# Kernel optimization log

Measured on AMD Instinct MI355X. Metric: run time of the kernel, lower is better.

Reference implementation:

```python
import jax, jax.numpy as jnp
import numpy as np

CHUNK = 512
LR = 0.001  # fast-weight learning_rate


def setup_inputs() -> dict:
    key = jax.random.key(0)
    k1, k2, k3, k4 = jax.random.split(key, 4)
    B, S, H, F = 4, 4096, 1024, 4096
    x = jax.random.normal(k1, (B, S, H), dtype=jnp.float32)
    w0 = jax.random.normal(k2, (H, F), dtype=jnp.float32) * 0.02
    w1 = jax.random.normal(k3, (F, H), dtype=jnp.float32) * 0.02
    w2 = jax.random.normal(k4, (H, F), dtype=jnp.float32) * 0.02
    return {"x": x, "w0": w0, "w1": w1, "w2": w2}


def _fast_weight(xc, a0, a1, a2):
    # SwiGLU fast-weight MLP (LaCT-style): [B,C,H] -> [B,C,H]
    h = jax.nn.silu(jnp.einsum('bch,hf->bcf', xc, a0)) * jnp.einsum('bch,hf->bcf', xc, a2)
    return jnp.einsum('bcf,fh->bch', h, a1)


def reference(x, w0, w1, w2):
    B, S, H = x.shape
    nC = S // CHUNK
    # [nC, B, CHUNK, H] so scan iterates over chunks
    xc = x.reshape(B, nC, CHUNK, H).transpose(1, 0, 2, 3)

    def step(carry, x_chunk):
        a0, a1, a2, acc_loss = carry
        out = _fast_weight(x_chunk, a0, a1, a2)
        chunk_loss = jnp.mean((out - x_chunk) ** 2)
        decay = 1.0 - LR * chunk_loss  # per-chunk scalar weight decay
        return (a0 * decay, a1 * decay, a2 * decay, acc_loss + chunk_loss), out

    init = (w0, w1, w2, jnp.float32(0.0))
    (_, _, _, total_loss), outs = jax.lax.scan(step, init, xc)
    output = outs.transpose(1, 0, 2, 3).reshape(B, S, H)
    return output, total_loss / nC
```

## Files before the change

kernel.cpp:

```cpp
#include <hip/hip_runtime.h>

typedef float f32x4 __attribute__((ext_vector_type(4)));
typedef short bf16x8 __attribute__((ext_vector_type(8)));
typedef unsigned short u16;

#define B_SZ 4
#define S_SZ 4096
#define H_SZ 1024
#define F_SZ 4096
#define CHUNK_SZ 512
#define NCHUNK 8
#define MCH 2048
#define LRATE 0.001f
#define NSPLIT 4

__device__ __forceinline__ u16 f2bf(float f) {
  unsigned u = __float_as_uint(f);
  u += 0x7FFFu + ((u >> 16) & 1u);
  return (u16)(u >> 16);
}
__device__ __forceinline__ float bf2f(u16 u) {
  return __uint_as_float(((unsigned)u) << 16);
}

__device__ __forceinline__ void gload_lds16(const void* g, void* l) {
  __builtin_amdgcn_global_load_lds(
      (const __attribute__((address_space(1))) unsigned int*)g,
      (__attribute__((address_space(3))) unsigned int*)l, 16, 0, 0);
}


__global__ __launch_bounds__(256) void k_init(float* scal) {
  if (threadIdx.x == 0) { scal[0] = 1.f; scal[1] = 0.f; }
}

__global__ __launch_bounds__(256) void k_cvt_x(const float* __restrict__ x,
                                               u16* __restrict__ xb) {
  size_t i = ((size_t)blockIdx.x * 256 + threadIdx.x) * 8;
  float4 v0 = *(const float4*)(x + i);
  float4 v1 = *(const float4*)(x + i + 4);
  union { u16 u[8]; bf16x8 v; } o;
  o.u[0] = f2bf(v0.x); o.u[1] = f2bf(v0.y); o.u[2] = f2bf(v0.z); o.u[3] = f2bf(v0.w);
  o.u[4] = f2bf(v1.x); o.u[5] = f2bf(v1.y); o.u[6] = f2bf(v1.z); o.u[7] = f2bf(v1.w);
  *(bf16x8*)(xb + i) = o.v;
}

__global__ __launch_bounds__(256) void k_transpose_cvt(const float* __restrict__ W,
                                                       u16* __restrict__ Wt,
                                                       int R, int C) {
  __shared__ float tile[32][33];
  int tx = threadIdx.x & 31, ty = threadIdx.x >> 5;
  int r0 = blockIdx.y << 5, c0 = blockIdx.x << 5;
#pragma unroll
  for (int i = 0; i < 4; i++)
    tile[ty + i * 8][tx] = W[(size_t)(r0 + ty + i * 8) * C + c0 + tx];
  __syncthreads();
#pragma unroll
  for (int i = 0; i < 4; i++)
    Wt[(size_t)(c0 + ty + i * 8) * R + r0 + tx] = f2bf(tile[tx][ty + i * 8]);
}

__global__ __launch_bounds__(256, 2) void k_gemm_gu(
    const u16* __restrict__ xb,
    const u16* __restrict__ w0t,
    const u16* __restrict__ w2t,
    u16* __restrict__ hbuf,
    const float* __restrict__ scal, int chunk) {
  __shared__ __align__(16) u16 sA[128 * 64];
  __shared__ __align__(16) u16 sB0[128 * 64];
  __shared__ __align__(16) u16 sB2[128 * 64];

  int t = threadIdx.x;
  int lane = t & 63, wid = t >> 6;
  int wm = wid >> 1, wn = wid & 1;

  int orig = blockIdx.x + (gridDim.x * blockIdx.y);
  int nwg = gridDim.x * gridDim.y;
  int wg = (orig & 7) * (nwg >> 3) + (orig >> 3);
  int tm = wg & 15, tn = wg >> 4;

  int gm0 = tm << 7;
  int bb = gm0 >> 9;
  int pos0 = gm0 & 511;
  const u16* Abase = xb + ((size_t)bb * S_SZ + (size_t)chunk * CHUNK_SZ + pos0) * H_SZ;

  int srow = t >> 3;
  int scol = (((t & 7) ^ (srow & 7)) << 3);
  const u16* aSrc  = Abase + (size_t)srow * H_SZ + scol;
  const u16* b0Src = w0t + ((size_t)(tn << 7) + srow) * H_SZ + scol;
  const u16* b2Src = w2t + ((size_t)(tn << 7) + srow) * H_SZ + scol;
  char* aDst  = (char*)sA  + t * 16;
  char* b0Dst = (char*)sB0 + t * 16;
  char* b2Dst = (char*)sB2 + t * 16;

  f32x4 acc0[4][4], acc2[4][4];
#pragma unroll
  for (int i = 0; i < 4; i++)
#pragma unroll
    for (int j = 0; j < 4; j++)
#pragma unroll
      for (int k = 0; k < 4; k++) { acc0[i][j][k] = 0.f; acc2[i][j][k] = 0.f; }

  int arow = (wm << 6) + (lane & 15);
  int brow = (wn << 6) + (lane & 15);
  int sl0 = (lane >> 4) ^ (lane & 7);
  int sl1 = ((lane >> 4) | 4) ^ (lane & 7);
  const int aO0 = arow * 128 + sl0 * 16, aO1 = arow * 128 + sl1 * 16;
  const int bO0 = brow * 128 + sl0 * 16, bO1 = brow * 128 + sl1 * 16;

#pragma unroll 1
  for (int k0 = 0; k0 < H_SZ; k0 += 64) {
#pragma unroll
    for (int r = 0; r < 4; r++) {
      gload_lds16(aSrc  + (size_t)r * 32 * H_SZ, aDst  + r * 4096);
      gload_lds16(b0Src + (size_t)r * 32 * H_SZ, b0Dst + r * 4096);
      gload_lds16(b2Src + (size_t)r * 32 * H_SZ, b2Dst + r * 4096);
    }
    aSrc += 64; b0Src += 64; b2Src += 64;
    __syncthreads();

    {
      bf16x8 av[4], b0v[4], b2v[4];
#pragma unroll
      for (int fr = 0; fr < 4; fr++) av[fr] = *(const bf16x8*)((const char*)sA + aO0 + fr * 2048);
#pragma unroll
      for (int fc = 0; fc < 4; fc++) {
        b0v[fc] = *(const bf16x8*)((const char*)sB0 + bO0 + fc * 2048);
        b2v[fc] = *(const bf16x8*)((const char*)sB2 + bO0 + fc * 2048);
      }
#pragma unroll
      for (int fr = 0; fr < 4; fr++)
#pragma unroll
        for (int fc = 0; fc < 4; fc++) {
          acc0[fr][fc] = __builtin_amdgcn_mfma_f32_16x16x32_bf16(av[fr], b0v[fc], acc0[fr][fc], 0, 0, 0);
          acc2[fr][fc] = __builtin_amdgcn_mfma_f32_16x16x32_bf16(av[fr], b2v[fc], acc2[fr][fc], 0, 0, 0);
        }
    }
    {
      bf16x8 av[4], b0v[4], b2v[4];
#pragma unroll
      for (int fr = 0; fr < 4; fr++) av[fr] = *(const bf16x8*)((const char*)sA + aO1 + fr * 2048);
#pragma unroll
      for (int fc = 0; fc < 4; fc++) {
        b0v[fc] = *(const bf16x8*)((const char*)sB0 + bO1 + fc * 2048);
        b2v[fc] = *(const bf16x8*)((const char*)sB2 + bO1 + fc * 2048);
      }
#pragma unroll
      for (int fr = 0; fr < 4; fr++)
#pragma unroll
        for (int fc = 0; fc < 4; fc++) {
          acc0[fr][fc] = __builtin_amdgcn_mfma_f32_16x16x32_bf16(av[fr], b0v[fc], acc0[fr][fc], 0, 0, 0);
          acc2[fr][fc] = __builtin_amdgcn_mfma_f32_16x16x32_bf16(av[fr], b2v[fc], acc2[fr][fc], 0, 0, 0);
        }
    }
    __syncthreads();
  }

  float D = scal[0];
#pragma unroll
  for (int fr = 0; fr < 4; fr++)
#pragma unroll
    for (int fc = 0; fc < 4; fc++) {
      int row0 = (tm << 7) + (wm << 6) + (fr << 4) + ((lane >> 4) << 2);
      int col = (tn << 7) + (wn << 6) + (fc << 4) + (lane & 15);
#pragma unroll
      for (int j = 0; j < 4; j++) {
        float g = D * acc0[fr][fc][j];
        float u = D * acc2[fr][fc][j];
        float sil = g / (1.f + __expf(-g));
        hbuf[(size_t)(row0 + j) * F_SZ + col] = f2bf(sil * u);
      }
    }
}

__global__ __launch_bounds__(256, 2) void k_gemm_out(
    const u16* __restrict__ hbuf,
    const u16* __restrict__ w1t,
    u16* __restrict__ pbuf) {
  __shared__ __align__(16) u16 sA[128 * 64];
  __shared__ __align__(16) u16 sB[128 * 64];

  int t = threadIdx.x;
  int lane = t & 63, wid = t >> 6;
  int wm = wid >> 1, wn = wid & 1;

  int orig = blockIdx.x + gridDim.x * (blockIdx.y + gridDim.y * blockIdx.z);
  int nwg = gridDim.x * gridDim.y * gridDim.z;
  int wg = (orig & 7) * (nwg >> 3) + (orig >> 3);
  int tm = wg & 15;
  int tn = (wg >> 4) & 7;
  int kz = wg >> 7;

  int srow = t >> 3;
  int scol = (((t & 7) ^ (srow & 7)) << 3);
  const u16* aSrc = hbuf + ((size_t)(tm << 7) + srow) * F_SZ + kz * 1024 + scol;
  const u16* bSrc = w1t + ((size_t)(tn << 7) + srow) * F_SZ + kz * 1024 + scol;
  char* aDst = (char*)sA + t * 16;
  char* bDst = (char*)sB + t * 16;

  f32x4 acc[4][4];
#pragma unroll
  for (int i = 0; i < 4; i++)
#pragma unroll
    for (int j = 0; j < 4; j++)
#pragma unroll
      for (int k = 0; k < 4; k++) acc[i][j][k] = 0.f;

  int arow = (wm << 6) + (lane & 15);
  int brow = (wn << 6) + (lane & 15);
  int sl0 = (lane >> 4) ^ (lane & 7);
  int sl1 = ((lane >> 4) | 4) ^ (lane & 7);
  const int aO0 = arow * 128 + sl0 * 16, aO1 = arow * 128 + sl1 * 16;
  const int bO0 = brow * 128 + sl0 * 16, bO1 = brow * 128 + sl1 * 16;

#pragma unroll 1
  for (int k0 = 0; k0 < 1024; k0 += 64) {
#pragma unroll
    for (int r = 0; r < 4; r++) {
      gload_lds16(aSrc + (size_t)r * 32 * F_SZ, aDst + r * 4096);
      gload_lds16(bSrc + (size_t)r * 32 * F_SZ, bDst + r * 4096);
    }
    aSrc += 64; bSrc += 64;
    __syncthreads();

    {
      bf16x8 av[4], bv[4];
#pragma unroll
      for (int fr = 0; fr < 4; fr++) av[fr] = *(const bf16x8*)((const char*)sA + aO0 + fr * 2048);
#pragma unroll
      for (int fc = 0; fc < 4; fc++) bv[fc] = *(const bf16x8*)((const char*)sB + bO0 + fc * 2048);
#pragma unroll
      for (int fr = 0; fr < 4; fr++)
#pragma unroll
        for (int fc = 0; fc < 4; fc++)
          acc[fr][fc] = __builtin_amdgcn_mfma_f32_16x16x32_bf16(av[fr], bv[fc], acc[fr][fc], 0, 0, 0);
    }
    {
      bf16x8 av[4], bv[4];
#pragma unroll
      for (int fr = 0; fr < 4; fr++) av[fr] = *(const bf16x8*)((const char*)sA + aO1 + fr * 2048);
#pragma unroll
      for (int fc = 0; fc < 4; fc++) bv[fc] = *(const bf16x8*)((const char*)sB + bO1 + fc * 2048);
#pragma unroll
      for (int fr = 0; fr < 4; fr++)
#pragma unroll
        for (int fc = 0; fc < 4; fc++)
          acc[fr][fc] = __builtin_amdgcn_mfma_f32_16x16x32_bf16(av[fr], bv[fc], acc[fr][fc], 0, 0, 0);
    }
    __syncthreads();
  }

#pragma unroll
  for (int fr = 0; fr < 4; fr++)
#pragma unroll
    for (int fc = 0; fc < 4; fc++) {
      int row0 = (tm << 7) + (wm << 6) + (fr << 4) + ((lane >> 4) << 2);
      int col = (tn << 7) + (wn << 6) + (fc << 4) + (lane & 15);
#pragma unroll
      for (int j = 0; j < 4; j++)
        pbuf[((size_t)kz * MCH + row0 + j) * 1024 + col] = f2bf(acc[fr][fc][j]);
    }
}

__global__ __launch_bounds__(256) void k_epilogue(
    const u16* __restrict__ pbuf, const float* __restrict__ x,
    float* __restrict__ out, const float* __restrict__ scal,
    float* __restrict__ partials, int chunk) {
  __shared__ float red[256];
  int t = threadIdx.x;
  size_t base = ((size_t)blockIdx.x * 256 + t) * 8;
  int row = (int)(base >> 10);
  int col = (int)(base & 1023);
  float D = scal[0];

  float s[8] = {0.f, 0.f, 0.f, 0.f, 0.f, 0.f, 0.f, 0.f};
#pragma unroll
  for (int kz = 0; kz < NSPLIT; kz++) {
    union { bf16x8 v; u16 u[8]; } p;
    p.v = *(const bf16x8*)(pbuf + (size_t)kz * MCH * 1024 + base);
#pragma unroll
    for (int j = 0; j < 8; j++) s[j] += bf2f(p.u[j]);
  }

  int bb = row >> 9, pos = row & 511;
  size_t off = ((size_t)bb * S_SZ + (size_t)chunk * CHUNK_SZ + pos) * H_SZ + col;
  float4 x0 = *(const float4*)(x + off);
  float4 x1 = *(const float4*)(x + off + 4);
  float xv[8] = {x0.x, x0.y, x0.z, x0.w, x1.x, x1.y, x1.z, x1.w};
  float ov[8];
  float psum = 0.f;
#pragma unroll
  for (int j = 0; j < 8; j++) {
    ov[j] = D * s[j];
    float e = ov[j] - xv[j];
    psum += e * e;
  }
  *(float4*)(out + off) = make_float4(ov[0], ov[1], ov[2], ov[3]);
  *(float4*)(out + off + 4) = make_float4(ov[4], ov[5], ov[6], ov[7]);

  red[t] = psum;
  __syncthreads();
  for (int s2 = 128; s2 > 0; s2 >>= 1) {
    if (t < s2) red[t] += red[t + s2];
    __syncthreads();
  }
  if (t == 0) partials[blockIdx.x] = red[0];
}

__global__ __launch_bounds__(256) void k_update(float* scal, const float* __restrict__ partials,
                                                float* lossout, int chunk) {
  __shared__ float red[256];
  int t = threadIdx.x;
  float s = 0.f;
  for (int i = t; i < 1024; i += 256) s += partials[i];
  red[t] = s;
  __syncthreads();
  for (int s2 = 128; s2 > 0; s2 >>= 1) {
    if (t < s2) red[t] += red[t + s2];
    __syncthreads();
  }
  if (t == 0) {
    float loss = red[0] / (float)((size_t)MCH * H_SZ);
    float total = scal[1] + loss;
    scal[1] = total;
    scal[0] = scal[0] * (1.f - LRATE * loss);
    if (chunk == NCHUNK - 1) lossout[0] = total / (float)NCHUNK;
  }
}

extern "C" void kernel_launch(void* const* d_in, const int* in_sizes, int n_in,
                              void* d_out, int out_size, void* d_ws, size_t ws_size,
                              hipStream_t stream) {
  const float* x = (const float*)d_in[0];
  const float* w0 = (const float*)d_in[1];
  const float* w1 = (const float*)d_in[2];
  const float* w2 = (const float*)d_in[3];
  float* out = (float*)d_out;

  char* ws = (char*)d_ws;
  float* scal = (float*)ws;
  float* partials = (float*)(ws + 1024);
  u16* xb = (u16*)(ws + 8192);
  u16* w0t = xb + (size_t)B_SZ * S_SZ * H_SZ;
  u16* w2t = w0t + (size_t)H_SZ * F_SZ;
  u16* w1t = w2t + (size_t)H_SZ * F_SZ;
  u16* hbuf = w1t + (size_t)F_SZ * H_SZ;
  u16* pbuf = hbuf + (size_t)MCH * F_SZ;

  k_init<<<1, 256, 0, stream>>>(scal);
  k_cvt_x<<<(B_SZ * S_SZ * H_SZ) / (256 * 8), 256, 0, stream>>>(x, xb);
  k_transpose_cvt<<<dim3(F_SZ / 32, H_SZ / 32), 256, 0, stream>>>(w0, w0t, H_SZ, F_SZ);
  k_transpose_cvt<<<dim3(H_SZ / 32, F_SZ / 32), 256, 0, stream>>>(w1, w1t, F_SZ, H_SZ);
  k_transpose_cvt<<<dim3(F_SZ / 32, H_SZ / 32), 256, 0, stream>>>(w2, w2t, H_SZ, F_SZ);

  float* lossout = out + (size_t)B_SZ * S_SZ * H_SZ;
  for (int c = 0; c < NCHUNK; c++) {
    k_gemm_gu<<<dim3(16, 32), 256, 0, stream>>>(xb, w0t, w2t, hbuf, scal, c);
    k_gemm_out<<<dim3(16, 8, NSPLIT), 256, 0, stream>>>(hbuf, w1t, pbuf);
    k_epilogue<<<1024, 256, 0, stream>>>(pbuf, x, out, scal, partials, c);
    k_update<<<1, 256, 0, stream>>>(scal, partials, lossout, c);
  }
}
```

Baseline: 571.3 us.

## Interleave gate/up weights and use 256x256 8-wave double-buffered GEMM

The gate and up projection weights are interleaved row-wise into a single combined matrix, so one GEMM with 256x256 tiles computes both. Neighbouring lanes are then paired with shuffles to apply SiLU*up. The kernel switches to 512 threads with double-buffered LDS, direct global-to-LDS loads issued between MFMA phases, explicit vmcnt waits, barriers and setprio. This is meant to overlap loads with compute and raise arithmetic intensity per tile. It uses 128KB of LDS per block, which limits occupancy, and only 256 blocks are launched.

```diff
diff --git a/kernel.cpp b/kernel.cpp
--- a/kernel.cpp
+++ b/kernel.cpp
@@ -29,6 +29,12 @@
       (__attribute__((address_space(3))) unsigned int*)l, 16, 0, 0);
 }
 
+#define VMCNT(n) asm volatile("s_waitcnt vmcnt(" #n ")" ::: "memory")
+#define SBAR() __builtin_amdgcn_s_barrier()
+#define SCHED_FENCE() __builtin_amdgcn_sched_barrier(0)
+#define PRIO1() __builtin_amdgcn_s_setprio(1)
+#define PRIO0() __builtin_amdgcn_s_setprio(0)
+
 
 __global__ __launch_bounds__(256) void k_init(float* scal) {
   if (threadIdx.x == 0) { scal[0] = 1.f; scal[1] = 0.f; }
@@ -47,7 +53,7 @@
 
 __global__ __launch_bounds__(256) void k_transpose_cvt(const float* __restrict__ W,
                                                        u16* __restrict__ Wt,
-                                                       int R, int C) {
+                                                       int R, int C, int rstride, int roff) {
   __shared__ float tile[32][33];
   int tx = threadIdx.x & 31, ty = threadIdx.x >> 5;
   int r0 = blockIdx.y << 5, c0 = blockIdx.x << 5;
@@ -57,118 +63,130 @@
   __syncthreads();
 #pragma unroll
   for (int i = 0; i < 4; i++)
-    Wt[(size_t)(c0 + ty + i * 8) * R + r0 + tx] = f2bf(tile[tx][ty + i * 8]);
-}
-
-__global__ __launch_bounds__(256, 2) void k_gemm_gu(
+    Wt[((size_t)(c0 + ty + i * 8) * rstride + roff) * R + r0 + tx] = f2bf(tile[tx][ty + i * 8]);
+}
+
+__global__ __launch_bounds__(512, 2) void k_gemm_gu8(
     const u16* __restrict__ xb,
-    const u16* __restrict__ w0t,
-    const u16* __restrict__ w2t,
+    const u16* __restrict__ wgu,
     u16* __restrict__ hbuf,
     const float* __restrict__ scal, int chunk) {
-  __shared__ __align__(16) u16 sA[128 * 64];
-  __shared__ __align__(16) u16 sB0[128 * 64];
-  __shared__ __align__(16) u16 sB2[128 * 64];
+  __shared__ __align__(16) u16 sA[32768];
+  __shared__ __align__(16) u16 sB[32768];
 
   int t = threadIdx.x;
   int lane = t & 63, wid = t >> 6;
-  int wm = wid >> 1, wn = wid & 1;
-
-  int orig = blockIdx.x + (gridDim.x * blockIdx.y);
-  int nwg = gridDim.x * gridDim.y;
-  int wg = (orig & 7) * (nwg >> 3) + (orig >> 3);
-  int tm = wg & 15, tn = wg >> 4;
-
-  int gm0 = tm << 7;
+  int wm = wid >> 2, wn = wid & 3;
+
+  int orig = blockIdx.x;
+  int wg = (orig & 7) * 32 + (orig >> 3);
+  int tn = wg >> 3, tm = wg & 7;
+
+  int gm0 = tm << 8;
   int bb = gm0 >> 9;
   int pos0 = gm0 & 511;
   const u16* Abase = xb + ((size_t)bb * S_SZ + (size_t)chunk * CHUNK_SZ + pos0) * H_SZ;
 
-  int srow = t >> 3;
-  int scol = (((t & 7) ^ (srow & 7)) << 3);
-  const u16* aSrc  = Abase + (size_t)srow * H_SZ + scol;
-  const u16* b0Src = w0t + ((size_t)(tn << 7) + srow) * H_SZ + scol;
-  const u16* b2Src = w2t + ((size_t)(tn << 7) + srow) * H_SZ + scol;
-  char* aDst  = (char*)sA  + t * 16;
-  char* b0Dst = (char*)sB0 + t * 16;
-  char* b2Dst = (char*)sB2 + t * 16;
-
-  f32x4 acc0[4][4], acc2[4][4];
-#pragma unroll
-  for (int i = 0; i < 4; i++)
+  int scol = (((t & 3) ^ ((t >> 3) & 3)) << 3);
+  const u16* aS = Abase + (size_t)(t >> 2) * H_SZ + scol;
+  const u16* bS = wgu + ((size_t)(tn << 8) + (t >> 2)) * H_SZ + scol;
+
+  f32x4 acc[8][4];
+#pragma unroll
+  for (int i = 0; i < 8; i++)
 #pragma unroll
     for (int j = 0; j < 4; j++)
 #pragma unroll
-      for (int k = 0; k < 4; k++) { acc0[i][j][k] = 0.f; acc2[i][j][k] = 0.f; }
-
-  int arow = (wm << 6) + (lane & 15);
-  int brow = (wn << 6) + (lane & 15);
-  int sl0 = (lane >> 4) ^ (lane & 7);
-  int sl1 = ((lane >> 4) | 4) ^ (lane & 7);
-  const int aO0 = arow * 128 + sl0 * 16, aO1 = arow * 128 + sl1 * 16;
-  const int bO0 = brow * 128 + sl0 * 16, bO1 = brow * 128 + sl1 * 16;
+      for (int k = 0; k < 4; k++) acc[i][j][k] = 0.f;
+
+  const int rslB = (((lane >> 4)) ^ (((lane & 15) >> 1) & 3)) * 16;
+  const int aRowB = ((wm << 7) + (lane & 15)) * 64 + rslB;
+  const int bRowB = ((wn << 6) + (lane & 15)) * 64 + rslB;
+
+#define STA(b_, kt_, ks_) {                                                  \
+    const u16* s_ = aS + (size_t)(kt_) * 64 + (ks_) * 32;                    \
+    char* d_ = (char*)sA + (b_) * 32768 + (ks_) * 16384 + t * 16;            \
+    gload_lds16(s_, d_);                                                     \
+    gload_lds16(s_ + (size_t)128 * H_SZ, d_ + 8192); }
+#define STB(b_, kt_, ks_) {                                                  \
+    const u16* s_ = bS + (size_t)(kt_) * 64 + (ks_) * 32;                    \
+    char* d_ = (char*)sB + (b_) * 32768 + (ks_) * 16384 + t * 16;            \
+    gload_lds16(s_, d_);                                                     \
+    gload_lds16(s_ + (size_t)128 * H_SZ, d_ + 8192); }
+
+#define LDA4(b_, ks_, FRS_) { _Pragma("unroll")                              \
+    for (int i_ = 0; i_ < 4; i_++)                                           \
+      av[i_] = *(const bf16x8*)((const char*)sA + (b_) * 32768 +             \
+                                (ks_) * 16384 + aRowB + (FRS_ + i_) * 1024); }
+#define LDB4(b_, ks_) { _Pragma("unroll")                                    \
+    for (int j_ = 0; j_ < 4; j_++)                                           \
+      bv[j_] = *(const bf16x8*)((const char*)sB + (b_) * 32768 +             \
+                                (ks_) * 16384 + bRowB + j_ * 1024); }
+
+#define MFMA16(FRS_) { _Pragma("unroll")                                     \
+    for (int i_ = 0; i_ < 4; i_++)                                           \
+      _Pragma("unroll")                                                      \
+      for (int j_ = 0; j_ < 4; j_++)                                         \
+        acc[FRS_ + i_][j_] = __builtin_amdgcn_mfma_f32_16x16x32_bf16(        \
+            av[i_], bv[j_], acc[FRS_ + i_][j_], 0, 0, 0); }
+
+#define TILE(b_, ktn_, ST_) {                                                \
+    bf16x8 av[4], bv[4];                                                     \
+                            \
+    LDA4(b_, 0, 0); LDB4(b_, 0);                                             \
+    if (ST_) STA(b_ ^ 1, ktn_, 0);                                           \
+    SBAR(); SCHED_FENCE();                                                   \
+    PRIO1(); MFMA16(0); PRIO0();                                             \
+    SBAR();                                                                  \
+                                  \
+    LDA4(b_, 0, 4);                                                          \
+    if (ST_) STB(b_ ^ 1, ktn_, 0);                                           \
+    SBAR(); SCHED_FENCE();                                                   \
+    PRIO1(); MFMA16(4); PRIO0();                                             \
+    if (ST_) { VMCNT(4); } else { VMCNT(0); }                                \
+    SBAR();                                                                  \
+                                                  \
+    LDA4(b_, 1, 0); LDB4(b_, 1);                                             \
+    if (ST_) STA(b_ ^ 1, ktn_, 1);                                           \
+    SBAR(); SCHED_FENCE();                                                   \
+    PRIO1(); MFMA16(0); PRIO0();                                             \
+    SBAR();                                                                  \
+                                                  \
+    LDA4(b_, 1, 4);                                                          \
+    if (ST_) STB(b_ ^ 1, ktn_, 1);                                           \
+    SBAR(); SCHED_FENCE();                                                   \
+    PRIO1(); MFMA16(4); PRIO0();                                             \
+    if (ST_) { VMCNT(4); SBAR(); }                                           \
+  }
+
+  STA(0, 0, 0); STB(0, 0, 0); STA(0, 0, 1); STB(0, 0, 1);
+  VMCNT(4);
+  SBAR();
 
 #pragma unroll 1
-  for (int k0 = 0; k0 < H_SZ; k0 += 64) {
-#pragma unroll
-    for (int r = 0; r < 4; r++) {
-      gload_lds16(aSrc  + (size_t)r * 32 * H_SZ, aDst  + r * 4096);
-      gload_lds16(b0Src + (size_t)r * 32 * H_SZ, b0Dst + r * 4096);
-      gload_lds16(b2Src + (size_t)r * 32 * H_SZ, b2Dst + r * 4096);
-    }
-    aSrc += 64; b0Src += 64; b2Src += 64;
-    __syncthreads();
-
-    {
-      bf16x8 av[4], b0v[4], b2v[4];
-#pragma unroll
-      for (int fr = 0; fr < 4; fr++) av[fr] = *(const bf16x8*)((const char*)sA + aO0 + fr * 2048);
-#pragma unroll
-      for (int fc = 0; fc < 4; fc++) {
-        b0v[fc] = *(const bf16x8*)((const char*)sB0 + bO0 + fc * 2048);
-        b2v[fc] = *(const bf16x8*)((const char*)sB2 + bO0 + fc * 2048);
-      }
-#pragma unroll
-      for (int fr = 0; fr < 4; fr++)
-#pragma unroll
-        for (int fc = 0; fc < 4; fc++) {
-          acc0[fr][fc] = __builtin_amdgcn_mfma_f32_16x16x32_bf16(av[fr], b0v[fc], acc0[fr][fc], 0, 0, 0);
-          acc2[fr][fc] = __builtin_amdgcn_mfma_f32_16x16x32_bf16(av[fr], b2v[fc], acc2[fr][fc], 0, 0, 0);
-        }
-    }
-    {
-      bf16x8 av[4], b0v[4], b2v[4];
-#pragma unroll
-      for (int fr = 0; fr < 4; fr++) av[fr] = *(const bf16x8*)((const char*)sA + aO1 + fr * 2048);
-#pragma unroll
-      for (int fc = 0; fc < 4; fc++) {
-        b0v[fc] = *(const bf16x8*)((const char*)sB0 + bO1 + fc * 2048);
-        b2v[fc] = *(const bf16x8*)((const char*)sB2 + bO1 + fc * 2048);
-      }
-#pragma unroll
-      for (int fr = 0; fr < 4; fr++)
-#pragma unroll
-        for (int fc = 0; fc < 4; fc++) {
-          acc0[fr][fc] = __builtin_amdgcn_mfma_f32_16x16x32_bf16(av[fr], b0v[fc], acc0[fr][fc], 0, 0, 0);
-          acc2[fr][fc] = __builtin_amdgcn_mfma_f32_16x16x32_bf16(av[fr], b2v[fc], acc2[fr][fc], 0, 0, 0);
-        }
-    }
-    __syncthreads();
-  }
+  for (int kt = 0; kt < 14; kt += 2) {
+    TILE(0, kt + 1, 1);
+    TILE(1, kt + 2, 1);
+  }
+  TILE(0, 15, 1);
+  TILE(1, 0, 0);
 
   float D = scal[0];
 #pragma unroll
-  for (int fr = 0; fr < 4; fr++)
+  for (int fr = 0; fr < 8; fr++)
 #pragma unroll
     for (int fc = 0; fc < 4; fc++) {
-      int row0 = (tm << 7) + (wm << 6) + (fr << 4) + ((lane >> 4) << 2);
-      int col = (tn << 7) + (wn << 6) + (fc << 4) + (lane & 15);
+      int row0 = (tm << 8) + (wm << 7) + (fr << 4) + ((lane >> 4) << 2);
+      int col = (tn << 8) + (wn << 6) + (fc << 4) + (lane & 15);
+      int f = col >> 1;
 #pragma unroll
       for (int j = 0; j < 4; j++) {
-        float g = D * acc0[fr][fc][j];
-        float u = D * acc2[fr][fc][j];
-        float sil = g / (1.f + __expf(-g));
-        hbuf[(size_t)(row0 + j) * F_SZ + col] = f2bf(sil * u);
+        float v = acc[fr][fc][j];
+        float w = __shfl_xor(v, 1);
+        float g = D * ((lane & 1) ? w : v);
+        float u = D * ((lane & 1) ? v : w);
+        float h = (g / (1.f + __expf(-g))) * u;
+        if (!(lane & 1)) hbuf[(size_t)(row0 + j) * F_SZ + f] = f2bf(h);
       }
     }
 }
@@ -341,21 +359,20 @@
   float* scal = (float*)ws;
   float* partials = (float*)(ws + 1024);
   u16* xb = (u16*)(ws + 8192);
-  u16* w0t = xb + (size_t)B_SZ * S_SZ * H_SZ;
-  u16* w2t = w0t + (size_t)H_SZ * F_SZ;
-  u16* w1t = w2t + (size_t)H_SZ * F_SZ;
+  u16* wgu = xb + (size_t)B_SZ * S_SZ * H_SZ;
+  u16* w1t = wgu + (size_t)8192 * 1024;
   u16* hbuf = w1t + (size_t)F_SZ * H_SZ;
   u16* pbuf = hbuf + (size_t)MCH * F_SZ;
 
   k_init<<<1, 256, 0, stream>>>(scal);
   k_cvt_x<<<(B_SZ * S_SZ * H_SZ) / (256 * 8), 256, 0, stream>>>(x, xb);
-  k_transpose_cvt<<<dim3(F_SZ / 32, H_SZ / 32), 256, 0, stream>>>(w0, w0t, H_SZ, F_SZ);
-  k_transpose_cvt<<<dim3(H_SZ / 32, F_SZ / 32), 256, 0, stream>>>(w1, w1t, F_SZ, H_SZ);
-  k_transpose_cvt<<<dim3(F_SZ / 32, H_SZ / 32), 256, 0, stream>>>(w2, w2t, H_SZ, F_SZ);
+  k_transpose_cvt<<<dim3(F_SZ / 32, H_SZ / 32), 256, 0, stream>>>(w0, wgu, H_SZ, F_SZ, 2, 0);
+  k_transpose_cvt<<<dim3(F_SZ / 32, H_SZ / 32), 256, 0, stream>>>(w2, wgu, H_SZ, F_SZ, 2, 1);
+  k_transpose_cvt<<<dim3(H_SZ / 32, F_SZ / 32), 256, 0, stream>>>(w1, w1t, F_SZ, H_SZ, 1, 0);
 
   float* lossout = out + (size_t)B_SZ * S_SZ * H_SZ;
   for (int c = 0; c < NCHUNK; c++) {
-    k_gemm_gu<<<dim3(16, 32), 256, 0, stream>>>(xb, w0t, w2t, hbuf, scal, c);
+    k_gemm_gu8<<<dim3(256), 512, 0, stream>>>(xb, wgu, hbuf, scal, c);
     k_gemm_out<<<dim3(16, 8, NSPLIT), 256, 0, stream>>>(hbuf, w1t, pbuf);
     k_epilogue<<<1024, 256, 0, stream>>>(pbuf, x, out, scal, partials, c);
     k_update<<<1, 256, 0, stream>>>(scal, partials, lossout, c);
```

Result: slower. 652.2 us (+14.2%).
